# Kernel optimization log

Hardware: AMD Instinct MI355X
Metric: run time of the kernel (lower is better)

The kernel has to match this reference:

```python
import jax, jax.numpy as jnp
import numpy as np

N_NODES = 50000
N_EDGES = 600000
D = 128            # out_feats
N_ETYPES = 4
N_STEPS = 5


def setup_inputs() -> dict:
    key = jax.random.key(0)
    ks = jax.random.split(key, 10)
    h = jax.random.normal(ks[0], (N_NODES, D), dtype=jnp.float32)
    src = jax.random.randint(ks[1], (N_EDGES,), 0, N_NODES)
    dst = jax.random.randint(ks[2], (N_EDGES,), 0, N_NODES)
    # rel_type values are 1..n_etypes in the original module
    etypes = jax.random.randint(ks[3], (N_EDGES,), 1, N_ETYPES + 1)
    s = 1.0 / np.sqrt(D)
    # per-edge-type Linear(out_feats, out_feats): y = x @ W.T + b
    W_lin = jax.random.normal(ks[4], (N_ETYPES, D, D), dtype=jnp.float32) * s
    b_lin = jnp.zeros((N_ETYPES, D), dtype=jnp.float32)
    # GRUCell params (torch layout: rows ordered r, z, n)
    w_ih = jax.random.uniform(ks[5], (3 * D, D), minval=-s, maxval=s, dtype=jnp.float32)
    w_hh = jax.random.uniform(ks[6], (3 * D, D), minval=-s, maxval=s, dtype=jnp.float32)
    b_ih = jax.random.uniform(ks[7], (3 * D,), minval=-s, maxval=s, dtype=jnp.float32)
    b_hh = jax.random.uniform(ks[8], (3 * D,), minval=-s, maxval=s, dtype=jnp.float32)
    return {"h": h, "src": src, "dst": dst, "etypes": etypes,
            "W_lin": W_lin, "b_lin": b_lin,
            "w_ih": w_ih, "w_hh": w_hh, "b_ih": b_ih, "b_hh": b_hh}


def _gru_cell(a, h, w_ih, w_hh, b_ih, b_hh):
    gi = a @ w_ih.T + b_ih          # [N, 3D]
    gh = h @ w_hh.T + b_hh          # [N, 3D]
    i_r, i_z, i_n = jnp.split(gi, 3, axis=-1)
    h_r, h_z, h_n = jnp.split(gh, 3, axis=-1)
    r = jax.nn.sigmoid(i_r + h_r)
    z = jax.nn.sigmoid(i_z + h_z)
    n = jnp.tanh(i_n + r * h_n)
    return (1.0 - z) * n + z * h


def reference(h, src, dst, etypes, W_lin, b_lin, w_ih, w_hh, b_ih, b_hh):
    N = h.shape[0]
    et = etypes - 1                 # 0-based edge type index
    for _ in range(N_STEPS):
        # per-type node transforms: t[k] = h @ W_lin[k].T + b_lin[k]  -> [K, N, D]
        t = jnp.einsum('nd,kfd->knf', h, W_lin) + b_lin[:, None, :]
        msg = t[et, src]            # gather per-edge transformed source feats [E, D]
        a = jax.ops.segment_sum(msg, dst, num_segments=N)  # scatter-sum aggregation
        h = _gru_cell(a, h, w_ih, w_hh, b_ih, b_hh)
    return h
```

## Files before the change

### kernel.cpp

```cpp
#include <hip/hip_runtime.h>
#include <hip/hip_bf16.h>
#include <cstdint>
#include <cstddef>

#define N_NODES 50000
#define N_EDGES 600000
#define DF 128
#define N_ETYPES 4
#define N_STEPS 5
#define SCAN_NB 196
#define GRU_TILES 3125
#define GRU_BLOCKS 256
#define LIN_BLOCKS 256
#define TSTRIDE 136
#define OSTR 76
#define FILL_CHUNKS 2344
#define FILL_RANGE (N_NODES / 8)

typedef _Float16 f16x8 __attribute__((ext_vector_type(8)));
typedef _Float16 f16x4 __attribute__((ext_vector_type(4)));
typedef float f32x4 __attribute__((ext_vector_type(4)));

__device__ __forceinline__ float sigmoid_fast(float x) {
    return 1.0f / (1.0f + __expf(-x));
}
__device__ __forceinline__ float tanh_fast(float x) {
    return 1.0f - 2.0f / (__expf(2.0f * x) + 1.0f);
}


__global__ __launch_bounds__(256) void k_setup(
    const float* __restrict__ Wl, const float* __restrict__ wih,
    const float* __restrict__ whh, const float* __restrict__ h,
    const int* __restrict__ dst,
    _Float16* __restrict__ Wl_h, _Float16* __restrict__ Bc,
    _Float16* __restrict__ hh, int* __restrict__ deg) {
    int i = blockIdx.x * 256 + threadIdx.x;
    if (i < N_ETYPES * DF * DF * 3 / 2) {
        if (i < N_ETYPES * DF * DF) Wl_h[i] = (_Float16)Wl[i];
        int row = i >> 8;
        int k = i & 255;
        float v = (k < 128) ? wih[row * 128 + k] : whh[row * 128 + (k - 128)];
        Bc[i] = (_Float16)v;
    }
    if (i < N_NODES * DF / 4) {
        float4 v = ((const float4*)h)[i];
        f16x4 o;
        o.x = (_Float16)v.x; o.y = (_Float16)v.y;
        o.z = (_Float16)v.z; o.w = (_Float16)v.w;
        ((f16x4*)hh)[i] = o;
    }
    if (i < N_EDGES) atomicAdd(&deg[dst[i]], 1);
}

__global__ __launch_bounds__(256) void k_part(
    const int* __restrict__ deg, int* __restrict__ part, int N) {
    __shared__ int s[256];
    int t = threadIdx.x, i = blockIdx.x * 256 + t;
    s[t] = (i < N) ? deg[i] : 0;
    __syncthreads();
    for (int off = 128; off > 0; off >>= 1) {
        if (t < off) s[t] += s[t + off];
        __syncthreads();
    }
    if (t == 0) part[blockIdx.x] = s[0];
}

__global__ __launch_bounds__(256) void k_scan1(int* __restrict__ part, int nb) {
    __shared__ int s[256];
    int t = threadIdx.x;
    int v = (t < nb) ? part[t] : 0;
    s[t] = v;
    __syncthreads();
    for (int off = 1; off < 256; off <<= 1) {
        int u = (t >= off) ? s[t - off] : 0;
        __syncthreads();
        s[t] += u;
        __syncthreads();
    }
    if (t < nb) part[t] = s[t] - v;
}

__global__ __launch_bounds__(256) void k_row(
    const int* __restrict__ deg, const int* __restrict__ part,
    int* __restrict__ row_start, int* __restrict__ cursor, int N) {
    __shared__ int s[256];
    int t = threadIdx.x, i = blockIdx.x * 256 + t;
    int d = (i < N) ? deg[i] : 0;
    s[t] = d;
    __syncthreads();
    for (int off = 1; off < 256; off <<= 1) {
        int u = (t >= off) ? s[t - off] : 0;
        __syncthreads();
        s[t] += u;
        __syncthreads();
    }
    int rs = part[blockIdx.x] + s[t] - d;
    if (i < N) {
        row_start[i] = rs;
        cursor[i] = rs;
        if (i == N - 1) row_start[N] = rs + d;
    }
}

__global__ __launch_bounds__(256) void k_fill(
    const int* __restrict__ src, const int* __restrict__ dst,
    const int* __restrict__ ety, int* __restrict__ cursor,
    int* __restrict__ csr, int E) {
    const int range = blockIdx.x & 7;
    const int chunk = blockIdx.x >> 3;
    const int e = chunk * 256 + threadIdx.x;
    const int lo = range * FILL_RANGE;
    const int hi = lo + FILL_RANGE;
    if (e < E) {
        int d = dst[e];
        if (d >= lo && d < hi) {
            int slot = atomicAdd(&cursor[d], 1);
            csr[slot] = src[e] | ((ety[e] - 1) << 16);
        }
    }
}


__global__ __launch_bounds__(1024) void k_lin(
    const _Float16* __restrict__ hh, const _Float16* __restrict__ Wl,
    const float* __restrict__ b_lin, _Float16* __restrict__ t_out, int N) {
    __shared__ _Float16 O[2][N_ETYPES * 16 * TSTRIDE];
    __shared__ __align__(16) char Ast[4][4096];
    const int wave = threadIdx.x >> 6, lane = threadIdx.x & 63;
    const int col16 = lane & 15, quad = lane >> 4;
    const int g = wave >> 2;
    const int s = wave & 3;

    f16x8 b[2][4];
#pragma unroll
    for (int ct = 0; ct < 2; ct++) {
        const _Float16* bp = Wl + (size_t)g * DF * DF
                           + (size_t)(s * 32 + ct * 16 + col16) * DF + quad * 8;
#pragma unroll
        for (int kt = 0; kt < 4; kt++) b[ct][kt] = *(const f16x8*)(bp + kt * 32);
    }
    const float bias0 = b_lin[g * DF + s * 32 + col16];
    const float bias1 = b_lin[g * DF + s * 32 + 16 + col16];

    const int olocal = (wave & 3) * 1024 + lane * 16;
    const int oswl = olocal ^ (((olocal >> 8) & 7) << 4);
    const int abase = col16 * 256 + quad * 16;
    const int axor = (col16 & 7) << 4;

    auto STAGE = [&](int iter) {
        if (wave < 4) {
            int tt = blockIdx.x + iter * LIN_BLOCKS;
            if (tt >= GRU_TILES) tt = GRU_TILES - 1;
            const char* gp = (const char*)hh + (size_t)tt * 4096 + oswl;
            char* lp = &Ast[iter & 3][(wave & 3) * 1024];
            __builtin_amdgcn_global_load_lds(
                (const __attribute__((address_space(1))) void*)gp,
                (__attribute__((address_space(3))) void*)lp, 16, 0, 0);
        }
    };

    const int ek = threadIdx.x >> 8;
    const int erow = (threadIdx.x & 255) >> 4;
    const int ec8 = threadIdx.x & 15;

    STAGE(0);
    STAGE(1);
    asm volatile("s_waitcnt vmcnt(1)" ::: "memory");
    __builtin_amdgcn_s_barrier();
    __builtin_amdgcn_sched_barrier(0);

    int it = 0;
    for (int tile = blockIdx.x; tile < GRU_TILES; tile += LIN_BLOCKS, ++it) {
        const int r0 = tile * 16;
        STAGE(it + 2);

        const char* As = (const char*)Ast[it & 3];
        _Float16* Ob = O[it & 1];

        f16x8 A[4];
#pragma unroll
        for (int kt = 0; kt < 4; kt++) {
            int off = (abase + kt * 64) ^ axor;
            A[kt] = *(const f16x8*)(As + off);
        }

        f32x4 acc0 = {0.f, 0.f, 0.f, 0.f}, acc1 = {0.f, 0.f, 0.f, 0.f};
#pragma unroll
        for (int kt = 0; kt < 4; kt++) {
            acc0 = __builtin_amdgcn_mfma_f32_16x16x32_f16(A[kt], b[0][kt], acc0, 0, 0, 0);
            acc1 = __builtin_amdgcn_mfma_f32_16x16x32_f16(A[kt], b[1][kt], acc1, 0, 0, 0);
        }

        _Float16* Og = Ob + g * (16 * TSTRIDE);
#pragma unroll
        for (int i = 0; i < 4; i++) {
            Og[(quad * 4 + i) * TSTRIDE + s * 32 + col16] = (_Float16)(acc0[i] + bias0);
            Og[(quad * 4 + i) * TSTRIDE + s * 32 + 16 + col16] = (_Float16)(acc1[i] + bias1);
        }

        asm volatile("s_waitcnt vmcnt(1) lgkmcnt(0)" ::: "memory");
        __builtin_amdgcn_s_barrier();
        __builtin_amdgcn_sched_barrier(0);

        f16x8 v = *(const f16x8*)&Ob[ek * (16 * TSTRIDE) + erow * TSTRIDE + ec8 * 8];
        *(f16x8*)(t_out + ((size_t)ek * N + (r0 + erow)) * DF + ec8 * 8) = v;
    }
    asm volatile("s_waitcnt vmcnt(0)" ::: "memory");
}

__global__ __launch_bounds__(256) void k_agg(
    const _Float16* __restrict__ t, const int* __restrict__ row_start,
    const int* __restrict__ csr, _Float16* __restrict__ ah, int N) {
    const int wave = threadIdx.x >> 6, lane = threadIdx.x & 63;
    const int g4 = lane >> 4;
    const int c8 = lane & 15;
    const int n = blockIdx.x * 4 + wave;
    const int beg = row_start[n], end = row_start[n + 1];
    float acc[8] = {0.f, 0.f, 0.f, 0.f, 0.f, 0.f, 0.f, 0.f};
    for (int e = beg; e < end; e += 16) {
        int i0 = e + g4, i1 = e + 4 + g4, i2 = e + 8 + g4, i3 = e + 12 + g4;
        float m0 = (i0 < end) ? 1.0f : 0.0f;
        float m1 = (i1 < end) ? 1.0f : 0.0f;
        float m2 = (i2 < end) ? 1.0f : 0.0f;
        float m3 = (i3 < end) ? 1.0f : 0.0f;
        int j0 = (i0 < end) ? i0 : end - 1;
        int j1 = (i1 < end) ? i1 : end - 1;
        int j2 = (i2 < end) ? i2 : end - 1;
        int j3 = (i3 < end) ? i3 : end - 1;
        int p0 = csr[j0], p1 = csr[j1], p2 = csr[j2], p3 = csr[j3];
        f16x8 x0 = *(const f16x8*)(t + ((((size_t)(p0 >> 16)) * N + (p0 & 0xFFFF)) << 7) + c8 * 8);
        f16x8 x1 = *(const f16x8*)(t + ((((size_t)(p1 >> 16)) * N + (p1 & 0xFFFF)) << 7) + c8 * 8);
        f16x8 x2 = *(const f16x8*)(t + ((((size_t)(p2 >> 16)) * N + (p2 & 0xFFFF)) << 7) + c8 * 8);
        f16x8 x3 = *(const f16x8*)(t + ((((size_t)(p3 >> 16)) * N + (p3 & 0xFFFF)) << 7) + c8 * 8);
#pragma unroll
        for (int j = 0; j < 8; j++) acc[j] += m0 * (float)x0[j];
#pragma unroll
        for (int j = 0; j < 8; j++) acc[j] += m1 * (float)x1[j];
#pragma unroll
        for (int j = 0; j < 8; j++) acc[j] += m2 * (float)x2[j];
#pragma unroll
        for (int j = 0; j < 8; j++) acc[j] += m3 * (float)x3[j];
    }
#pragma unroll
    for (int j = 0; j < 8; j++) {
        acc[j] += __shfl_xor(acc[j], 32, 64);
        acc[j] += __shfl_xor(acc[j], 16, 64);
    }
    if (lane < 16) {
        f16x8 o;
#pragma unroll
        for (int j = 0; j < 8; j++) o[j] = (_Float16)acc[j];
        *(f16x8*)(ah + ((size_t)n << 7) + c8 * 8) = o;
    }
}

__global__ __launch_bounds__(512) void k_grulin(
    const _Float16* __restrict__ ah, const _Float16* __restrict__ hh,
    const _Float16* __restrict__ Bc, const float* __restrict__ b_ih,
    const float* __restrict__ b_hh, const _Float16* __restrict__ Wl,
    const float* __restrict__ b_lin, _Float16* __restrict__ hh_next,
    _Float16* __restrict__ t_out, float* __restrict__ out_f32, int N) {
    __shared__ __align__(16) char Ast[4][8192];
    __shared__ __align__(16) char Hn[2][4096];
    __shared__ _Float16 Ow[8][16 * OSTR];
    const int wave = threadIdx.x >> 6, lane = threadIdx.x & 63;
    const int col16 = lane & 15, quad = lane >> 4;
    const int c = wave * 16 + col16;

    f16x8 br[8], bz[8], bi[4], bh[4];
    {
        const _Float16* Br = Bc + ((size_t)c << 8);
        const _Float16* Bz = Bc + ((size_t)(128 + c) << 8);
        const _Float16* Bn = Bc + ((size_t)(256 + c) << 8);
#pragma unroll
        for (int kt = 0; kt < 8; kt++) {
            br[kt] = *(const f16x8*)(Br + kt * 32 + quad * 8);
            bz[kt] = *(const f16x8*)(Bz + kt * 32 + quad * 8);
        }
#pragma unroll
        for (int kt = 0; kt < 4; kt++) {
            bi[kt] = *(const f16x8*)(Bn + kt * 32 + quad * 8);
            bh[kt] = *(const f16x8*)(Bn + 128 + kt * 32 + quad * 8);
        }
    }
    const float bir = b_ih[c] + b_hh[c];
    const float biz = b_ih[128 + c] + b_hh[128 + c];
    const float bin_ = b_ih[256 + c];
    const float bhn_ = b_hh[256 + c];

    const int et = wave >> 1;
    const int ch64 = (wave & 1) * 64;
    f16x8 wl[4][4];
    float blv[4];
#pragma unroll
    for (int ct = 0; ct < 4; ct++) {
        const _Float16* wp = Wl + (size_t)et * DF * DF
                           + (size_t)(ch64 + ct * 16 + col16) * DF + quad * 8;
#pragma unroll
        for (int kt = 0; kt < 4; kt++) wl[ct][kt] = *(const f16x8*)(wp + kt * 32);
        blv[ct] = b_lin[et * DF + ch64 + ct * 16 + col16];
    }

    const int olocal = (wave & 3) * 1024 + lane * 16;
    const int oswl = olocal ^ (((olocal >> 8) & 7) << 4);
    const char* sbase = (wave < 4) ? (const char*)ah : (const char*)hh;
    const int abase = col16 * 256 + quad * 16;
    const int axor = (col16 & 7) << 4;

    auto STAGE = [&](int iter) {
        int tt = blockIdx.x + iter * GRU_BLOCKS;
        if (tt >= GRU_TILES) tt = GRU_TILES - 1;
        const char* gp = sbase + (size_t)tt * 4096 + oswl;
        char* lp = &Ast[iter & 3][wave * 1024];
        __builtin_amdgcn_global_load_lds(
            (const __attribute__((address_space(1))) void*)gp,
            (__attribute__((address_space(3))) void*)lp, 16, 0, 0);
    };

    STAGE(0);
    STAGE(1);
    asm volatile("s_waitcnt vmcnt(1)" ::: "memory");
    __builtin_amdgcn_s_barrier();
    __builtin_amdgcn_sched_barrier(0);

    int it = 0;
    for (int tile = blockIdx.x; tile < GRU_TILES; tile += GRU_BLOCKS, ++it) {
        const int r0 = tile * 16;
        STAGE(it + 2);

        const char* As = (const char*)Ast[it & 3];

        f16x8 A[8];
#pragma unroll
        for (int kt = 0; kt < 8; kt++) {
            int off = ((kt & 4) << 10) + abase + (kt & 3) * 64;
            off ^= axor;
            A[kt] = *(const f16x8*)(As + off);
        }

        f32x4 ar = {0.f, 0.f, 0.f, 0.f}, az = {0.f, 0.f, 0.f, 0.f};
        f32x4 ai = {0.f, 0.f, 0.f, 0.f}, an = {0.f, 0.f, 0.f, 0.f};
#pragma unroll
        for (int kt = 0; kt < 8; kt++) {
            ar = __builtin_amdgcn_mfma_f32_16x16x32_f16(A[kt], br[kt], ar, 0, 0, 0);
            az = __builtin_amdgcn_mfma_f32_16x16x32_f16(A[kt], bz[kt], az, 0, 0, 0);
        }
#pragma unroll
        for (int kt = 0; kt < 4; kt++) {
            ai = __builtin_amdgcn_mfma_f32_16x16x32_f16(A[kt], bi[kt], ai, 0, 0, 0);
            an = __builtin_amdgcn_mfma_f32_16x16x32_f16(A[4 + kt], bh[kt], an, 0, 0, 0);
        }

        char* Hb = Hn[it & 1];
#pragma unroll
        for (int i = 0; i < 4; i++) {
            int row = quad * 4 + i;
            int hoff = (4096 + row * 256 + c * 2) ^ ((row & 7) << 4);
            float hprev = (float)*(const _Float16*)(As + hoff);
            float r = sigmoid_fast(ar[i] + bir);
            float z = sigmoid_fast(az[i] + biz);
            float nn = tanh_fast(ai[i] + bin_ + r * (an[i] + bhn_));
            float hv = (1.f - z) * nn + z * hprev;
            if (out_f32) {
                out_f32[((size_t)(r0 + row) << 7) + c] = hv;
            } else {
                *(_Float16*)(Hb + ((row * 256 + c * 2) ^ ((row & 7) << 4))) = (_Float16)hv;
            }
        }

        if (t_out) {
            asm volatile("s_waitcnt lgkmcnt(0)" ::: "memory");
            __builtin_amdgcn_s_barrier();
            __builtin_amdgcn_sched_barrier(0);

            f16x8 A2[4];
#pragma unroll
            for (int kt = 0; kt < 4; kt++) {
                int off = (col16 * 256 + kt * 64 + quad * 16) ^ ((col16 & 7) << 4);
                A2[kt] = *(const f16x8*)(Hb + off);
            }
#pragma unroll
            for (int ct = 0; ct < 4; ct++) {
                f32x4 acc = {0.f, 0.f, 0.f, 0.f};
#pragma unroll
                for (int kt = 0; kt < 4; kt++)
                    acc = __builtin_amdgcn_mfma_f32_16x16x32_f16(A2[kt], wl[ct][kt], acc, 0, 0, 0);
#pragma unroll
                for (int i = 0; i < 4; i++)
                    Ow[wave][(quad * 4 + i) * OSTR + ct * 16 + col16] = (_Float16)(acc[i] + blv[ct]);
            }
        }

        asm volatile("s_waitcnt vmcnt(1) lgkmcnt(0)" ::: "memory");
        __builtin_amdgcn_s_barrier();
        __builtin_amdgcn_sched_barrier(0);

        if (!out_f32) {
            int hrow = threadIdx.x >> 5, hch = threadIdx.x & 31;
            f16x4 hv4 = *(const f16x4*)(Hb + ((hrow * 256 + hch * 8) ^ ((hrow & 7) << 4)));
            *(f16x4*)(hh_next + ((size_t)(r0 + hrow) << 7) + hch * 4) = hv4;
        }
        if (t_out) {
#pragma unroll
            for (int j = 0; j < 2; j++) {
                int chunk = lane + 64 * j;
                int trow = chunk >> 3, c8 = chunk & 7;
                f16x8 v = *(const f16x8*)&Ow[wave][trow * OSTR + c8 * 8];
                *(f16x8*)(t_out + ((size_t)et * N + (r0 + trow)) * DF + ch64 + c8 * 8) = v;
            }
        }
    }
    asm volatile("s_waitcnt vmcnt(0)" ::: "memory");
}


extern "C" void kernel_launch(void* const* d_in, const int* in_sizes, int n_in,
                              void* d_out, int out_size, void* d_ws, size_t ws_size,
                              hipStream_t stream) {
    const float* h0    = (const float*)d_in[0];
    const int*   src   = (const int*)d_in[1];
    const int*   dst   = (const int*)d_in[2];
    const int*   ety   = (const int*)d_in[3];
    const float* W_lin = (const float*)d_in[4];
    const float* b_lin = (const float*)d_in[5];
    const float* w_ih  = (const float*)d_in[6];
    const float* w_hh  = (const float*)d_in[7];
    const float* b_ih  = (const float*)d_in[8];
    const float* b_hh  = (const float*)d_in[9];
    float* hout = (float*)d_out;

    char* p = (char*)d_ws;
    auto alloc = [&](size_t bytes) -> char* {
        char* r = p;
        p += (bytes + 255) & ~(size_t)255;
        return r;
    };
    _Float16* h_a    = (_Float16*)alloc((size_t)N_NODES * DF * 2);
    _Float16* h_b    = (_Float16*)alloc((size_t)N_NODES * DF * 2);
    _Float16* a_half = (_Float16*)alloc((size_t)N_NODES * DF * 2);
    _Float16* t_half = (_Float16*)alloc((size_t)N_ETYPES * N_NODES * DF * 2);
    _Float16* Wl_h   = (_Float16*)alloc((size_t)N_ETYPES * DF * DF * 2);
    _Float16* Bc     = (_Float16*)alloc((size_t)3 * DF * 2 * DF * 2);
    int* deg       = (int*)alloc((size_t)N_NODES * 4);
    int* row_start = (int*)alloc((size_t)(N_NODES + 1) * 4);
    int* cursor    = (int*)alloc((size_t)N_NODES * 4);
    int* csr       = (int*)alloc((size_t)N_EDGES * 4);
    int* part      = (int*)alloc((size_t)SCAN_NB * 4);

    hipMemsetAsync(deg, 0, (size_t)N_NODES * 4, stream);
    k_setup<<<(N_NODES * DF / 4 + 255) / 256, 256, 0, stream>>>(
        W_lin, w_ih, w_hh, h0, dst, Wl_h, Bc, h_a, deg);
    k_part<<<SCAN_NB, 256, 0, stream>>>(deg, part, N_NODES);
    k_scan1<<<1, 256, 0, stream>>>(part, SCAN_NB);
    k_row<<<SCAN_NB, 256, 0, stream>>>(deg, part, row_start, cursor, N_NODES);
    k_fill<<<FILL_CHUNKS * 8, 256, 0, stream>>>(src, dst, ety, cursor, csr, N_EDGES);

    _Float16* hc = h_a;
    _Float16* hn = h_b;
    k_lin<<<LIN_BLOCKS, 1024, 0, stream>>>(hc, Wl_h, b_lin, t_half, N_NODES);
    for (int s = 0; s < N_STEPS; s++) {
        k_agg<<<N_NODES / 4, 256, 0, stream>>>(t_half, row_start, csr, a_half, N_NODES);
        const bool last = (s == N_STEPS - 1);
        k_grulin<<<GRU_BLOCKS, 512, 0, stream>>>(
            a_half, hc, Bc, b_ih, b_hh, Wl_h, b_lin, hn,
            last ? nullptr : t_half, last ? hout : nullptr, N_NODES);
        _Float16* tmp = hc; hc = hn; hn = tmp;
    }
}
```

Baseline: 514.1 us.

## Software-pipeline per-type linear transform one tile behind GRU update

Defers the per-edge-type linear MFMA transform and the t_out/hh_next stores for a tile to the next loop iteration. It reads the previous tile's hidden state from the other half of the double-buffered Hn, which removes one LDS barrier per tile and lets the transform overlap with the next tile's GRU work. A drain step after the loop handles the last tile. In exchange it keeps more values live in registers across iterations, and the hh_next store now depends on t_out rather than on out_f32.

```diff
diff --git a/kernel.cpp b/kernel.cpp
--- a/kernel.cpp
+++ b/kernel.cpp
@@ -308,6 +308,10 @@
     const int abase = col16 * 256 + quad * 16;
     const int axor = (col16 & 7) << 4;
 
+    const int hrow = threadIdx.x >> 5, hch = threadIdx.x & 31;
+    const int trow0 = lane >> 3, tc80 = lane & 7;
+    const int trow1 = (lane + 64) >> 3, tc81 = (lane + 64) & 7;
+
     auto STAGE = [&](int iter) {
         int tt = blockIdx.x + iter * GRU_BLOCKS;
         if (tt >= GRU_TILES) tt = GRU_TILES - 1;
@@ -318,6 +322,33 @@
             (__attribute__((address_space(3))) void*)lp, 16, 0, 0);
     };
 
+    auto LIN = [&](const char* Hp, f16x8& tv0, f16x8& tv1, f16x4& hv4) {
+        f16x8 A2[4];
+#pragma unroll
+        for (int kt = 0; kt < 4; kt++) {
+            int off = (col16 * 256 + kt * 64 + quad * 16) ^ ((col16 & 7) << 4);
+            A2[kt] = *(const f16x8*)(Hp + off);
+        }
+#pragma unroll
+        for (int ct = 0; ct < 4; ct++) {
+            f32x4 acc = {0.f, 0.f, 0.f, 0.f};
+#pragma unroll
+            for (int kt = 0; kt < 4; kt++)
+                acc = __builtin_amdgcn_mfma_f32_16x16x32_f16(A2[kt], wl[ct][kt], acc, 0, 0, 0);
+#pragma unroll
+            for (int i = 0; i < 4; i++)
+                Ow[wave][(quad * 4 + i) * OSTR + ct * 16 + col16] = (_Float16)(acc[i] + blv[ct]);
+        }
+        tv0 = *(const f16x8*)&Ow[wave][trow0 * OSTR + tc80 * 8];
+        tv1 = *(const f16x8*)&Ow[wave][trow1 * OSTR + tc81 * 8];
+        hv4 = *(const f16x4*)(Hp + ((hrow * 256 + hch * 8) ^ ((hrow & 7) << 4)));
+    };
+    auto TSTORE = [&](int pr0, const f16x8& tv0, const f16x8& tv1, const f16x4& hv4) {
+        *(f16x8*)(t_out + ((size_t)et * N + (pr0 + trow0)) * DF + ch64 + tc80 * 8) = tv0;
+        *(f16x8*)(t_out + ((size_t)et * N + (pr0 + trow1)) * DF + ch64 + tc81 * 8) = tv1;
+        *(f16x4*)(hh_next + ((size_t)(pr0 + hrow) << 7) + hch * 4) = hv4;
+    };
+
     STAGE(0);
     STAGE(1);
     asm volatile("s_waitcnt vmcnt(1)" ::: "memory");
@@ -325,6 +356,9 @@
     __builtin_amdgcn_sched_barrier(0);
 
     int it = 0;
+    int prev_r0 = -1;
+    f16x8 tv0, tv1;
+    f16x4 hv4;
     for (int tile = blockIdx.x; tile < GRU_TILES; tile += GRU_BLOCKS, ++it) {
         const int r0 = tile * 16;
         STAGE(it + 2);
@@ -369,47 +403,18 @@
             }
         }
 
-        if (t_out) {
-            asm volatile("s_waitcnt lgkmcnt(0)" ::: "memory");
-            __builtin_amdgcn_s_barrier();
-            __builtin_amdgcn_sched_barrier(0);
-
-            f16x8 A2[4];
-#pragma unroll
-            for (int kt = 0; kt < 4; kt++) {
-                int off = (col16 * 256 + kt * 64 + quad * 16) ^ ((col16 & 7) << 4);
-                A2[kt] = *(const f16x8*)(Hb + off);
-            }
-#pragma unroll
-            for (int ct = 0; ct < 4; ct++) {
-                f32x4 acc = {0.f, 0.f, 0.f, 0.f};
-#pragma unroll
-                for (int kt = 0; kt < 4; kt++)
-                    acc = __builtin_amdgcn_mfma_f32_16x16x32_f16(A2[kt], wl[ct][kt], acc, 0, 0, 0);
-#pragma unroll
-                for (int i = 0; i < 4; i++)
-                    Ow[wave][(quad * 4 + i) * OSTR + ct * 16 + col16] = (_Float16)(acc[i] + blv[ct]);
-            }
-        }
+        if (t_out && prev_r0 >= 0) LIN((const char*)Hn[(it & 1) ^ 1], tv0, tv1, hv4);
 
         asm volatile("s_waitcnt vmcnt(1) lgkmcnt(0)" ::: "memory");
         __builtin_amdgcn_s_barrier();
         __builtin_amdgcn_sched_barrier(0);
 
-        if (!out_f32) {
-            int hrow = threadIdx.x >> 5, hch = threadIdx.x & 31;
-            f16x4 hv4 = *(const f16x4*)(Hb + ((hrow * 256 + hch * 8) ^ ((hrow & 7) << 4)));
-            *(f16x4*)(hh_next + ((size_t)(r0 + hrow) << 7) + hch * 4) = hv4;
-        }
-        if (t_out) {
-#pragma unroll
-            for (int j = 0; j < 2; j++) {
-                int chunk = lane + 64 * j;
-                int trow = chunk >> 3, c8 = chunk & 7;
-                f16x8 v = *(const f16x8*)&Ow[wave][trow * OSTR + c8 * 8];
-                *(f16x8*)(t_out + ((size_t)et * N + (r0 + trow)) * DF + ch64 + c8 * 8) = v;
-            }
-        }
+        if (t_out && prev_r0 >= 0) TSTORE(prev_r0, tv0, tv1, hv4);
+        prev_r0 = r0;
+    }
+    if (t_out && prev_r0 >= 0) {
+        LIN((const char*)Hn[(it & 1) ^ 1], tv0, tv1, hv4);
+        TSTORE(prev_r0, tv0, tv1, hv4);
     }
     asm volatile("s_waitcnt vmcnt(0)" ::: "memory");
 }
```

After: 523.1 us. Within noise of the previous version (+1.7%).

## Process two GRU tiles per iteration in fused GRU+linear kernel

Applied to the files above, without the earlier changes.

Restructures the k_grulin main loop to stage, compute and store two 16-row tiles per iteration, with a fixed trip count of six plus a tail tile. Doubling the Hn and Ow shared buffers halves the number of block-wide barriers and waits per tile, and gives more independent MFMA work between synchronisations. It also adds a launch-bounds occupancy hint of two blocks, which may force register pressure or spills given the many preloaded weight fragments. The hh_next store is now issued only when the linear output is written.

```diff
diff --git a/kernel.cpp b/kernel.cpp
--- a/kernel.cpp
+++ b/kernel.cpp
@@ -255,15 +255,15 @@
     }
 }
 
-__global__ __launch_bounds__(512) void k_grulin(
+__global__ __launch_bounds__(512, 2) void k_grulin(
     const _Float16* __restrict__ ah, const _Float16* __restrict__ hh,
     const _Float16* __restrict__ Bc, const float* __restrict__ b_ih,
     const float* __restrict__ b_hh, const _Float16* __restrict__ Wl,
     const float* __restrict__ b_lin, _Float16* __restrict__ hh_next,
     _Float16* __restrict__ t_out, float* __restrict__ out_f32, int N) {
     __shared__ __align__(16) char Ast[4][8192];
-    __shared__ __align__(16) char Hn[2][4096];
-    __shared__ _Float16 Ow[8][16 * OSTR];
+    __shared__ __align__(16) char Hn[2][2][4096];
+    __shared__ _Float16 Ow[8][2][16 * OSTR];
     const int wave = threadIdx.x >> 6, lane = threadIdx.x & 63;
     const int col16 = lane & 15, quad = lane >> 4;
     const int c = wave * 16 + col16;
@@ -308,29 +308,23 @@
     const int abase = col16 * 256 + quad * 16;
     const int axor = (col16 & 7) << 4;
 
-    auto STAGE = [&](int iter) {
-        int tt = blockIdx.x + iter * GRU_BLOCKS;
+    const int hrow = threadIdx.x >> 5, hch = threadIdx.x & 31;
+    const int trow0 = lane >> 3, tc80 = lane & 7;
+    const int trow1 = 8 + (lane >> 3), tc81 = lane & 7;
+
+    auto STAGE = [&](int tidx) {
+        int tt = blockIdx.x + tidx * GRU_BLOCKS;
         if (tt >= GRU_TILES) tt = GRU_TILES - 1;
         const char* gp = sbase + (size_t)tt * 4096 + oswl;
-        char* lp = &Ast[iter & 3][wave * 1024];
+        char* lp = &Ast[tidx & 3][wave * 1024];
         __builtin_amdgcn_global_load_lds(
             (const __attribute__((address_space(1))) void*)gp,
             (__attribute__((address_space(3))) void*)lp, 16, 0, 0);
     };
 
-    STAGE(0);
-    STAGE(1);
-    asm volatile("s_waitcnt vmcnt(1)" ::: "memory");
-    __builtin_amdgcn_s_barrier();
-    __builtin_amdgcn_sched_barrier(0);
-
-    int it = 0;
-    for (int tile = blockIdx.x; tile < GRU_TILES; tile += GRU_BLOCKS, ++it) {
-        const int r0 = tile * 16;
-        STAGE(it + 2);
-
-        const char* As = (const char*)Ast[it & 3];
-
+    auto GRUC = [&](int tidx, char* Hb) {
+        const int r0 = (blockIdx.x + tidx * GRU_BLOCKS) * 16;
+        const char* As = (const char*)Ast[tidx & 3];
         f16x8 A[8];
 #pragma unroll
         for (int kt = 0; kt < 8; kt++) {
@@ -338,7 +332,6 @@
             off ^= axor;
             A[kt] = *(const f16x8*)(As + off);
         }
-
         f32x4 ar = {0.f, 0.f, 0.f, 0.f}, az = {0.f, 0.f, 0.f, 0.f};
         f32x4 ai = {0.f, 0.f, 0.f, 0.f}, an = {0.f, 0.f, 0.f, 0.f};
 #pragma unroll
@@ -351,8 +344,6 @@
             ai = __builtin_amdgcn_mfma_f32_16x16x32_f16(A[kt], bi[kt], ai, 0, 0, 0);
             an = __builtin_amdgcn_mfma_f32_16x16x32_f16(A[4 + kt], bh[kt], an, 0, 0, 0);
         }
-
-        char* Hb = Hn[it & 1];
 #pragma unroll
         for (int i = 0; i < 4; i++) {
             int row = quad * 4 + i;
@@ -368,47 +359,74 @@
                 *(_Float16*)(Hb + ((row * 256 + c * 2) ^ ((row & 7) << 4))) = (_Float16)hv;
             }
         }
-
+    };
+
+    auto LINC = [&](const char* Hp, _Float16* Owb) {
+        f16x8 A2[4];
+#pragma unroll
+        for (int kt = 0; kt < 4; kt++) {
+            int off = (col16 * 256 + kt * 64 + quad * 16) ^ ((col16 & 7) << 4);
+            A2[kt] = *(const f16x8*)(Hp + off);
+        }
+#pragma unroll
+        for (int ct = 0; ct < 4; ct++) {
+            f32x4 acc = {0.f, 0.f, 0.f, 0.f};
+#pragma unroll
+            for (int kt = 0; kt < 4; kt++)
+                acc = __builtin_amdgcn_mfma_f32_16x16x32_f16(A2[kt], wl[ct][kt], acc, 0, 0, 0);
+#pragma unroll
+            for (int i = 0; i < 4; i++)
+                Owb[(quad * 4 + i) * OSTR + ct * 16 + col16] = (_Float16)(acc[i] + blv[ct]);
+        }
+    };
+
+    auto OSTORE = [&](int tidx, const char* Hp, const _Float16* Owb) {
+        const int r0 = (blockIdx.x + tidx * GRU_BLOCKS) * 16;
+        f16x8 tv0 = *(const f16x8*)&Owb[trow0 * OSTR + tc80 * 8];
+        f16x8 tv1 = *(const f16x8*)&Owb[trow1 * OSTR + tc81 * 8];
+        f16x4 hv4 = *(const f16x4*)(Hp + ((hrow * 256 + hch * 8) ^ ((hrow & 7) << 4)));
+        *(f16x8*)(t_out + ((size_t)et * N + (r0 + trow0)) * DF + ch64 + tc80 * 8) = tv0;
+        *(f16x8*)(t_out + ((size_t)et * N + (r0 + trow1)) * DF + ch64 + tc81 * 8) = tv1;
+        *(f16x4*)(hh_next + ((size_t)(r0 + hrow) << 7) + hch * 4) = hv4;
+    };
+
+    STAGE(0);
+    STAGE(1);
+    asm volatile("s_waitcnt vmcnt(0)" ::: "memory");
+    __builtin_amdgcn_s_barrier();
+    __builtin_amdgcn_sched_barrier(0);
+
+    for (int j = 0; j < 6; ++j) {
+        STAGE(2 * j + 2);
+        STAGE(2 * j + 3);
+        char* H0 = Hn[j & 1][0];
+        char* H1 = Hn[j & 1][1];
+        GRUC(2 * j, H0);
+        GRUC(2 * j + 1, H1);
         if (t_out) {
             asm volatile("s_waitcnt lgkmcnt(0)" ::: "memory");
             __builtin_amdgcn_s_barrier();
             __builtin_amdgcn_sched_barrier(0);
-
-            f16x8 A2[4];
-#pragma unroll
-            for (int kt = 0; kt < 4; kt++) {
-                int off = (col16 * 256 + kt * 64 + quad * 16) ^ ((col16 & 7) << 4);
-                A2[kt] = *(const f16x8*)(Hb + off);
-            }
-#pragma unroll
-            for (int ct = 0; ct < 4; ct++) {
-                f32x4 acc = {0.f, 0.f, 0.f, 0.f};
-#pragma unroll
-                for (int kt = 0; kt < 4; kt++)
-                    acc = __builtin_amdgcn_mfma_f32_16x16x32_f16(A2[kt], wl[ct][kt], acc, 0, 0, 0);
-#pragma unroll
-                for (int i = 0; i < 4; i++)
-                    Ow[wave][(quad * 4 + i) * OSTR + ct * 16 + col16] = (_Float16)(acc[i] + blv[ct]);
-            }
-        }
-
-        asm volatile("s_waitcnt vmcnt(1) lgkmcnt(0)" ::: "memory");
+            LINC(H0, Ow[wave][0]);
+            LINC(H1, Ow[wave][1]);
+        }
+        asm volatile("s_waitcnt vmcnt(0) lgkmcnt(0)" ::: "memory");
         __builtin_amdgcn_s_barrier();
         __builtin_amdgcn_sched_barrier(0);
-
-        if (!out_f32) {
-            int hrow = threadIdx.x >> 5, hch = threadIdx.x & 31;
-            f16x4 hv4 = *(const f16x4*)(Hb + ((hrow * 256 + hch * 8) ^ ((hrow & 7) << 4)));
-            *(f16x4*)(hh_next + ((size_t)(r0 + hrow) << 7) + hch * 4) = hv4;
-        }
         if (t_out) {
-#pragma unroll
-            for (int j = 0; j < 2; j++) {
-                int chunk = lane + 64 * j;
-                int trow = chunk >> 3, c8 = chunk & 7;
-                f16x8 v = *(const f16x8*)&Ow[wave][trow * OSTR + c8 * 8];
-                *(f16x8*)(t_out + ((size_t)et * N + (r0 + trow)) * DF + ch64 + c8 * 8) = v;
-            }
+            OSTORE(2 * j, H0, Ow[wave][0]);
+            OSTORE(2 * j + 1, H1, Ow[wave][1]);
+        }
+    }
+    if (blockIdx.x + 12 * GRU_BLOCKS < GRU_TILES) {
+        char* H0 = Hn[0][0];
+        GRUC(12, H0);
+        if (t_out) {
+            asm volatile("s_waitcnt lgkmcnt(0)" ::: "memory");
+            __builtin_amdgcn_s_barrier();
+            __builtin_amdgcn_sched_barrier(0);
+            LINC(H0, Ow[wave][0]);
+            OSTORE(12, H0, Ow[wave][0]);
         }
     }
     asm volatile("s_waitcnt vmcnt(0)" ::: "memory");
```

After: 514.6 us. About the same (+0.1%).

## Split GRU K-dimension across 16 waves and defer output stores to next tile

Applied to the files above, without the earlier changes.

The fused GRU+linear kernel now runs 1024 threads. Waves are split into two K-halves: one half handles the aggregated-message part, the other the hidden-state part. Partial gate sums are exchanged through LDS and combined by the second group. Stores of h_next and the per-type transformed features for the previous tile are deferred and issued by the first wave group while the next tile computes, which removes a barrier-serialised store phase. This adds an LDS round-trip and an extra barrier per tile, and raises register and LDS pressure at the larger block size.

```diff
diff --git a/kernel.cpp b/kernel.cpp
--- a/kernel.cpp
+++ b/kernel.cpp
@@ -13,7 +13,8 @@
 #define GRU_BLOCKS 256
 #define LIN_BLOCKS 256
 #define TSTRIDE 136
-#define OSTR 76
+#define XPSTR 17
+#define OSTR 40
 #define FILL_CHUNKS 2344
 #define FILL_RANGE (N_NODES / 8)
 
@@ -255,7 +256,7 @@
     }
 }
 
-__global__ __launch_bounds__(512) void k_grulin(
+__global__ __launch_bounds__(1024) void k_grulin(
     const _Float16* __restrict__ ah, const _Float16* __restrict__ hh,
     const _Float16* __restrict__ Bc, const float* __restrict__ b_ih,
     const float* __restrict__ b_hh, const _Float16* __restrict__ Wl,
@@ -263,25 +264,23 @@
     _Float16* __restrict__ t_out, float* __restrict__ out_f32, int N) {
     __shared__ __align__(16) char Ast[4][8192];
     __shared__ __align__(16) char Hn[2][4096];
-    __shared__ _Float16 Ow[8][16 * OSTR];
+    __shared__ float Xp[8][3][16 * XPSTR];
+    __shared__ _Float16 Ow[16][16 * OSTR];
     const int wave = threadIdx.x >> 6, lane = threadIdx.x & 63;
     const int col16 = lane & 15, quad = lane >> 4;
-    const int c = wave * 16 + col16;
-
-    f16x8 br[8], bz[8], bi[4], bh[4];
+    const int cg = wave & 7, kh = wave >> 3;
+    const int c = cg * 16 + col16;
+
+    f16x8 br[4], bz[4], bn[4];
     {
-        const _Float16* Br = Bc + ((size_t)c << 8);
-        const _Float16* Bz = Bc + ((size_t)(128 + c) << 8);
-        const _Float16* Bn = Bc + ((size_t)(256 + c) << 8);
-#pragma unroll
-        for (int kt = 0; kt < 8; kt++) {
+        const _Float16* Br = Bc + ((size_t)c << 8) + kh * 128;
+        const _Float16* Bz = Bc + ((size_t)(128 + c) << 8) + kh * 128;
+        const _Float16* Bn = Bc + ((size_t)(256 + c) << 8) + kh * 128;
+#pragma unroll
+        for (int kt = 0; kt < 4; kt++) {
             br[kt] = *(const f16x8*)(Br + kt * 32 + quad * 8);
             bz[kt] = *(const f16x8*)(Bz + kt * 32 + quad * 8);
-        }
-#pragma unroll
-        for (int kt = 0; kt < 4; kt++) {
-            bi[kt] = *(const f16x8*)(Bn + kt * 32 + quad * 8);
-            bh[kt] = *(const f16x8*)(Bn + 128 + kt * 32 + quad * 8);
+            bn[kt] = *(const f16x8*)(Bn + kt * 32 + quad * 8);
         }
     }
     const float bir = b_ih[c] + b_hh[c];
@@ -289,17 +288,17 @@
     const float bin_ = b_ih[256 + c];
     const float bhn_ = b_hh[256 + c];
 
-    const int et = wave >> 1;
-    const int ch64 = (wave & 1) * 64;
-    f16x8 wl[4][4];
-    float blv[4];
-#pragma unroll
-    for (int ct = 0; ct < 4; ct++) {
-        const _Float16* wp = Wl + (size_t)et * DF * DF
-                           + (size_t)(ch64 + ct * 16 + col16) * DF + quad * 8;
+    const int let = wave & 3;
+    const int cq32 = (wave >> 2) * 32;
+    f16x8 wl[2][4];
+    float blv[2];
+#pragma unroll
+    for (int ct = 0; ct < 2; ct++) {
+        const _Float16* wp = Wl + (size_t)let * DF * DF
+                           + (size_t)(cq32 + ct * 16 + col16) * DF + quad * 8;
 #pragma unroll
         for (int kt = 0; kt < 4; kt++) wl[ct][kt] = *(const f16x8*)(wp + kt * 32);
-        blv[ct] = b_lin[et * DF + ch64 + ct * 16 + col16];
+        blv[ct] = b_lin[let * DF + cq32 + ct * 16 + col16];
     }
 
     const int olocal = (wave & 3) * 1024 + lane * 16;
@@ -308,14 +307,32 @@
     const int abase = col16 * 256 + quad * 16;
     const int axor = (col16 & 7) << 4;
 
-    auto STAGE = [&](int iter) {
-        int tt = blockIdx.x + iter * GRU_BLOCKS;
-        if (tt >= GRU_TILES) tt = GRU_TILES - 1;
-        const char* gp = sbase + (size_t)tt * 4096 + oswl;
-        char* lp = &Ast[iter & 3][wave * 1024];
-        __builtin_amdgcn_global_load_lds(
-            (const __attribute__((address_space(1))) void*)gp,
-            (__attribute__((address_space(3))) void*)lp, 16, 0, 0);
+    const int hrow = threadIdx.x >> 5, hch = threadIdx.x & 31;
+
+    auto STAGE = [&](int tidx) {
+        if (wave < 8) {
+            int tt = blockIdx.x + tidx * GRU_BLOCKS;
+            if (tt >= GRU_TILES) tt = GRU_TILES - 1;
+            const char* gp = sbase + (size_t)tt * 4096 + oswl;
+            char* lp = &Ast[tidx & 3][wave * 1024];
+            __builtin_amdgcn_global_load_lds(
+                (const __attribute__((address_space(1))) void*)gp,
+                (__attribute__((address_space(3))) void*)lp, 16, 0, 0);
+        }
+    };
+
+    auto PSTORE = [&](int pr0, int prevpar) {
+        const char* Hp = (const char*)Hn[prevpar];
+        f16x4 hv4 = *(const f16x4*)(Hp + ((hrow * 256 + hch * 8) ^ ((hrow & 7) << 4)));
+        *(f16x4*)(hh_next + ((size_t)(pr0 + hrow) << 7) + hch * 4) = hv4;
+#pragma unroll
+        for (int j = 0; j < 2; j++) {
+            int chunk = (int)threadIdx.x + j * 512;
+            int w = chunk >> 6, r = (chunk >> 2) & 15, c8 = chunk & 3;
+            f16x8 tv = *(const f16x8*)&Ow[w][r * OSTR + c8 * 8];
+            *(f16x8*)(t_out + ((size_t)(w & 3) * N + (pr0 + r)) * DF
+                      + (w >> 2) * 32 + c8 * 8) = tv;
+        }
     };
 
     STAGE(0);
@@ -325,48 +342,64 @@
     __builtin_amdgcn_sched_barrier(0);
 
     int it = 0;
+    int prev_r0 = -1;
     for (int tile = blockIdx.x; tile < GRU_TILES; tile += GRU_BLOCKS, ++it) {
         const int r0 = tile * 16;
         STAGE(it + 2);
 
         const char* As = (const char*)Ast[it & 3];
 
-        f16x8 A[8];
-#pragma unroll
-        for (int kt = 0; kt < 8; kt++) {
-            int off = ((kt & 4) << 10) + abase + (kt & 3) * 64;
-            off ^= axor;
+        f16x8 A[4];
+#pragma unroll
+        for (int kt = 0; kt < 4; kt++) {
+            int off = (kh << 12) + ((abase + kt * 64) ^ axor);
             A[kt] = *(const f16x8*)(As + off);
         }
 
         f32x4 ar = {0.f, 0.f, 0.f, 0.f}, az = {0.f, 0.f, 0.f, 0.f};
-        f32x4 ai = {0.f, 0.f, 0.f, 0.f}, an = {0.f, 0.f, 0.f, 0.f};
-#pragma unroll
-        for (int kt = 0; kt < 8; kt++) {
+        f32x4 an = {0.f, 0.f, 0.f, 0.f};
+#pragma unroll
+        for (int kt = 0; kt < 4; kt++) {
             ar = __builtin_amdgcn_mfma_f32_16x16x32_f16(A[kt], br[kt], ar, 0, 0, 0);
             az = __builtin_amdgcn_mfma_f32_16x16x32_f16(A[kt], bz[kt], az, 0, 0, 0);
-        }
-#pragma unroll
-        for (int kt = 0; kt < 4; kt++) {
-            ai = __builtin_amdgcn_mfma_f32_16x16x32_f16(A[kt], bi[kt], ai, 0, 0, 0);
-            an = __builtin_amdgcn_mfma_f32_16x16x32_f16(A[4 + kt], bh[kt], an, 0, 0, 0);
-        }
-
-        char* Hb = Hn[it & 1];
-#pragma unroll
-        for (int i = 0; i < 4; i++) {
-            int row = quad * 4 + i;
-            int hoff = (4096 + row * 256 + c * 2) ^ ((row & 7) << 4);
-            float hprev = (float)*(const _Float16*)(As + hoff);
-            float r = sigmoid_fast(ar[i] + bir);
-            float z = sigmoid_fast(az[i] + biz);
-            float nn = tanh_fast(ai[i] + bin_ + r * (an[i] + bhn_));
-            float hv = (1.f - z) * nn + z * hprev;
-            if (out_f32) {
-                out_f32[((size_t)(r0 + row) << 7) + c] = hv;
-            } else {
-                *(_Float16*)(Hb + ((row * 256 + c * 2) ^ ((row & 7) << 4))) = (_Float16)hv;
+            an = __builtin_amdgcn_mfma_f32_16x16x32_f16(A[kt], bn[kt], an, 0, 0, 0);
+        }
+
+        if (kh == 0) {
+#pragma unroll
+            for (int i = 0; i < 4; i++) {
+                int row = quad * 4 + i;
+                Xp[cg][0][row * XPSTR + col16] = ar[i];
+                Xp[cg][1][row * XPSTR + col16] = az[i];
+                Xp[cg][2][row * XPSTR + col16] = an[i];
             }
+        }
+        asm volatile("s_waitcnt lgkmcnt(0)" ::: "memory");
+        __builtin_amdgcn_s_barrier();
+        __builtin_amdgcn_sched_barrier(0);
+
+        if (kh == 1) {
+            char* Hb = Hn[it & 1];
+#pragma unroll
+            for (int i = 0; i < 4; i++) {
+                int row = quad * 4 + i;
+                float pr = Xp[cg][0][row * XPSTR + col16];
+                float pz = Xp[cg][1][row * XPSTR + col16];
+                float pn = Xp[cg][2][row * XPSTR + col16];
+                float hprev = (float)*(const _Float16*)(
+                    As + 4096 + ((row * 256 + c * 2) ^ ((row & 7) << 4)));
+                float r = sigmoid_fast(pr + ar[i] + bir);
+                float z = sigmoid_fast(pz + az[i] + biz);
+                float nn = tanh_fast(pn + bin_ + r * (an[i] + bhn_));
+                float hv = (1.f - z) * nn + z * hprev;
+                if (out_f32) {
+                    out_f32[((size_t)(r0 + row) << 7) + c] = hv;
+                } else {
+                    *(_Float16*)(Hb + ((row * 256 + c * 2) ^ ((row & 7) << 4))) = (_Float16)hv;
+                }
+            }
+        } else if (t_out && prev_r0 >= 0) {
+            PSTORE(prev_r0, (it & 1) ^ 1);
         }
 
         if (t_out) {
@@ -374,6 +407,7 @@
             __builtin_amdgcn_s_barrier();
             __builtin_amdgcn_sched_barrier(0);
 
+            const char* Hb = (const char*)Hn[it & 1];
             f16x8 A2[4];
 #pragma unroll
             for (int kt = 0; kt < 4; kt++) {
@@ -381,35 +415,28 @@
                 A2[kt] = *(const f16x8*)(Hb + off);
             }
 #pragma unroll
-            for (int ct = 0; ct < 4; ct++) {
+            for (int ct = 0; ct < 2; ct++) {
                 f32x4 acc = {0.f, 0.f, 0.f, 0.f};
 #pragma unroll
                 for (int kt = 0; kt < 4; kt++)
                     acc = __builtin_amdgcn_mfma_f32_16x16x32_f16(A2[kt], wl[ct][kt], acc, 0, 0, 0);
 #pragma unroll
                 for (int i = 0; i < 4; i++)
-                    Ow[wave][(quad * 4 + i) * OSTR + ct * 16 + col16] = (_Float16)(acc[i] + blv[ct]);
+                    Ow[wave][(quad * 4 + i) * OSTR + ct * 16 + col16] =
+                        (_Float16)(acc[i] + blv[ct]);
             }
-        }
-
-        asm volatile("s_waitcnt vmcnt(1) lgkmcnt(0)" ::: "memory");
-        __builtin_amdgcn_s_barrier();
-        __builtin_amdgcn_sched_barrier(0);
-
-        if (!out_f32) {
-            int hrow = threadIdx.x >> 5, hch = threadIdx.x & 31;
-            f16x4 hv4 = *(const f16x4*)(Hb + ((hrow * 256 + hch * 8) ^ ((hrow & 7) << 4)));
-            *(f16x4*)(hh_next + ((size_t)(r0 + hrow) << 7) + hch * 4) = hv4;
-        }
-        if (t_out) {
-#pragma unroll
-            for (int j = 0; j < 2; j++) {
-                int chunk = lane + 64 * j;
-                int trow = chunk >> 3, c8 = chunk & 7;
-                f16x8 v = *(const f16x8*)&Ow[wave][trow * OSTR + c8 * 8];
-                *(f16x8*)(t_out + ((size_t)et * N + (r0 + trow)) * DF + ch64 + c8 * 8) = v;
-            }
-        }
+            asm volatile("s_waitcnt vmcnt(4) lgkmcnt(0)" ::: "memory");
+            __builtin_amdgcn_s_barrier();
+            __builtin_amdgcn_sched_barrier(0);
+        } else {
+            asm volatile("s_waitcnt vmcnt(1) lgkmcnt(0)" ::: "memory");
+            __builtin_amdgcn_s_barrier();
+            __builtin_amdgcn_sched_barrier(0);
+        }
+        prev_r0 = r0;
+    }
+    if (t_out && prev_r0 >= 0 && kh == 0) {
+        PSTORE(prev_r0, (it & 1) ^ 1);
     }
     asm volatile("s_waitcnt vmcnt(0)" ::: "memory");
 }
@@ -462,7 +489,7 @@
     for (int s = 0; s < N_STEPS; s++) {
         k_agg<<<N_NODES / 4, 256, 0, stream>>>(t_half, row_start, csr, a_half, N_NODES);
         const bool last = (s == N_STEPS - 1);
-        k_grulin<<<GRU_BLOCKS, 512, 0, stream>>>(
+        k_grulin<<<GRU_BLOCKS, 1024, 0, stream>>>(
             a_half, hc, Bc, b_ih, b_hh, Wl_h, b_lin, hn,
             last ? nullptr : t_half, last ? hout : nullptr, N_NODES);
         _Float16* tmp = hc; hc = hn; hn = tmp;
```

Result: slower. 551.6 us (+7.3%).
